# Kernel optimization log

Measured on AMD Instinct MI355X. Metric: run time of the kernel, lower is better.

## Reference

```python
import jax, jax.numpy as jnp
import numpy as np

NLAT, NLON = 361, 720
LMAX = NLAT               # equiangular grid: lmax = nlat
MMAX = NLON // 2 + 1      # mmax = nlon//2 + 1
B, C = 1, 128


def _precompute_legpoly(mmax, lmax, t, csphase=True):
    """Associated Legendre vandermonde P_l^m(cos t), orthonormal, inverse=True
    (norm factor 1 for 'ortho'). Shape [mmax, lmax, nlat]. Setup-time numpy only."""
    x = np.cos(t)
    nmax = max(mmax, lmax)
    vdm = np.zeros((nmax, nmax, len(x)))
    vdm[0, 0] = np.sqrt(1.0 / (4.0 * np.pi))
    for l in range(1, nmax):
        vdm[l - 1, l] = np.sqrt(2 * l + 1) * x * vdm[l - 1, l - 1]
        vdm[l, l] = np.sqrt((2 * l + 1) * (1 + x) * (1 - x) / (2 * l)) * vdm[l - 1, l - 1]
    for l in range(2, nmax):
        for m in range(l - 1):
            a = np.sqrt((2 * l - 1) / (l - m) * (2 * l + 1) / (l + m))
            b = np.sqrt((l + m - 1) / (l - m) * (2 * l + 1) / (2 * l - 3) * (l - m - 1) / (l + m))
            vdm[m, l] = a * x * vdm[m, l - 1] - b * vdm[m, l - 2]
    vdm = vdm[:mmax, :lmax]
    if csphase:
        vdm[1::2] *= -1.0  # Condon-Shortley phase on odd m
    return vdm


def setup_inputs() -> dict:
    key = jax.random.key(0)
    # spherical harmonic coefficients as real view: [B, C, lmax, mmax, 2]
    x_real = jax.random.normal(key, (B, C, LMAX, MMAX, 2), dtype=jnp.float32)
    # equiangular (Clenshaw-Curtiss) colatitudes, t = flip(arccos(cos(pi*j/(n-1))))
    t = np.pi * np.arange(NLAT) / (NLAT - 1)
    pct = jnp.asarray(_precompute_legpoly(MMAX, LMAX, t), dtype=jnp.float32)  # [mmax, lmax, nlat]
    return {"x_real": x_real, "pct": pct}


def reference(x_real, pct):
    # single-device case: comm sizes == 1, all distributed transposes are identity
    # and nlatpad == nlonpad == 0.
    # per-m triangular Legendre contraction over l (torch einsum '...lmr,mlk->...kmr')
    xs = jnp.einsum('bclmr,mlk->bckmr', x_real, pct)        # [B, C, nlat, mmax, 2]
    xc = jax.lax.complex(xs[..., 0], xs[..., 1])            # [B, C, nlat, mmax]
    # inverse real FFT along longitude, norm='forward' (no 1/n scaling on inverse)
    out = jnp.fft.irfft(xc, n=NLON, axis=-1, norm='forward')  # [B, C, nlat, nlon]
    return out.astype(x_real.dtype)
```

## Files before the change

### kernel.cpp

```cpp
#include <hip/hip_runtime.h>
#include <cstddef>

#define CC   128
#define LDIM 361
#define MDIM 361
#define KDIM 361
#define NLON 720
#define LP   384
#define MRP  736
#define NP   768
#define CK   (CC*KDIM)
#define CR   (2*CC)

typedef __attribute__((ext_vector_type(8))) short short8;
typedef __attribute__((ext_vector_type(4))) float floatx4;

__device__ __forceinline__ unsigned short f2bf(float f) {
    union { float f; unsigned u; } v; v.f = f;
    unsigned u = v.u;
    u += 0x7fffu + ((u >> 16) & 1u);
    return (unsigned short)(u >> 16);
}

__device__ __forceinline__ void async_copy16(const void* g, void* l) {
    __builtin_amdgcn_global_load_lds(
        (const __attribute__((address_space(1))) void*)g,
        (__attribute__((address_space(3))) void*)l, 16, 0, 0);
}

__global__ void sht_gen_T(unsigned short* __restrict__ Tp) {
    int idx = blockIdx.x * 256 + threadIdx.x;
    if (idx >= NP * MRP) return;
    int n = idx / MRP, mr = idx - n * MRP;
    float v = 0.f;
    if (n < NLON && mr < 2 * MDIM) {
        int m = mr >> 1, im = mr & 1;
        if (m == 0)            v = im ? 0.f : 1.f;
        else if (m == MDIM-1)  v = im ? 0.f : ((n & 1) ? -1.f : 1.f);
        else {
            int ph = (m * n) % NLON;
            float ang = (float)ph * (float)(3.14159265358979323846 / 360.0);
            v = im ? (-2.f * sinf(ang)) : (2.f * cosf(ang));
        }
    }
    Tp[idx] = f2bf(v);
}

__global__ __launch_bounds__(256)
void sht_prep_x(const float* __restrict__ x, unsigned short* __restrict__ xA) {
    __shared__ float2 tile[64][33];
    const int mt = blockIdx.x;
    const int lt = blockIdx.y;
    const int c  = blockIdx.z;
    const int t  = threadIdx.x;

    #pragma unroll
    for (int u = 0; u < 8; ++u) {
        int p  = t + 256 * u;
        int li = p >> 5, mi = p & 31;
        int l = lt * 64 + li, m = mt * 32 + mi;
        float2 v = make_float2(0.f, 0.f);
        if (l < LDIM && m < MDIM)
            v = *(const float2*)(x + ((size_t)(c * LDIM + l) * MDIM + m) * 2);
        tile[li][mi] = v;
    }
    __syncthreads();

    #pragma unroll
    for (int u = 0; u < 2; ++u) {
        int s  = t + 256 * u;
        int mi = s >> 4, rr = (s >> 3) & 1, lo = (s & 7) * 8;
        int m = mt * 32 + mi;
        if (m >= MDIM) continue;
        short8 h;
        #pragma unroll
        for (int e = 0; e < 8; ++e) {
            float2 p = tile[lo + e][mi];
            h[e] = (short)f2bf(rr ? p.y : p.x);
        }
        *(short8*)(xA + ((size_t)m * CR + 2 * c + rr) * LP + lt * 64 + lo) = h;
    }
}

__global__ __launch_bounds__(256)
void sht_stageA(const float* __restrict__ pct, const unsigned short* __restrict__ xA,
                unsigned short* __restrict__ xs) {
    __shared__ unsigned short As[128 * 32];
    __shared__ unsigned short Bs[32 * 130];

    const int m   = blockIdx.y;
    const int ct  = blockIdx.x & 1;
    const int kt  = blockIdx.x >> 1;
    const int c0  = ct * 128;
    const int n0  = kt * 128;
    const int t   = threadIdx.x;
    const int w   = t >> 6, L = t & 63;
    const int wr  = w & 1, wc = w >> 1;
    const int lane15 = L & 15, quad = L >> 4;
    const int bl = t >> 3, bkq = t & 7;

    const unsigned short* xAm = xA + (size_t)m * CR * LP;
    const float* pctm = pct + (size_t)m * LDIM * KDIM;

    floatx4 acc[4][4] = {};

    for (int kb = 0; kb < LP; kb += 32) {
        #pragma unroll
        for (int i = 0; i < 2; ++i) {
            int s = w * 128 + i * 64 + L;
            int cr = s >> 2, lq = s & 3;
            async_copy16(xAm + (size_t)(c0 + cr) * LP + kb + lq * 8,
                         As + (size_t)(w * 128 + i * 64) * 8);
        }
        {
            int l = kb + bl;
            bool lok = (l < LDIM);
            const float* prow = pctm + (size_t)l * KDIM;
            #pragma unroll
            for (int u = 0; u < 4; ++u) {
                int kc = n0 + u * 32 + bkq * 4;
                float f0 = (lok && kc + 0 < KDIM) ? prow[kc + 0] : 0.f;
                float f1 = (lok && kc + 1 < KDIM) ? prow[kc + 1] : 0.f;
                float f2 = (lok && kc + 2 < KDIM) ? prow[kc + 2] : 0.f;
                float f3 = (lok && kc + 3 < KDIM) ? prow[kc + 3] : 0.f;
                unsigned* bp = (unsigned*)&Bs[bl * 130 + u * 32 + bkq * 4];
                bp[0] = (unsigned)f2bf(f0) | ((unsigned)f2bf(f1) << 16);
                bp[1] = (unsigned)f2bf(f2) | ((unsigned)f2bf(f3) << 16);
            }
        }
        __syncthreads();

        short8 af[4];
        #pragma unroll
        for (int i = 0; i < 4; ++i) {
            int row = wr * 64 + i * 16 + lane15;
            af[i] = *(const short8*)&As[(row * 4 + quad) * 8];
        }
        #pragma unroll
        for (int jf = 0; jf < 4; ++jf) {
            int col = wc * 64 + jf * 16 + lane15;
            short8 bf;
            #pragma unroll
            for (int j = 0; j < 8; ++j)
                bf[j] = (short)Bs[(quad * 8 + j) * 130 + col];
            #pragma unroll
            for (int i = 0; i < 4; ++i)
                acc[i][jf] = __builtin_amdgcn_mfma_f32_16x16x32_bf16(af[i], bf, acc[i][jf], 0, 0, 0);
        }
        __syncthreads();
    }

    #pragma unroll
    for (int i = 0; i < 4; ++i) {
        #pragma unroll
        for (int jf = 0; jf < 4; ++jf) {
            int k = n0 + wc * 64 + jf * 16 + lane15;
            if (k >= KDIM) continue;
            #pragma unroll
            for (int eh = 0; eh < 2; ++eh) {
                int cr = c0 + wr * 64 + i * 16 + quad * 4 + eh * 2;
                int c  = cr >> 1;
                unsigned pack = (unsigned)f2bf(acc[i][jf][eh * 2]) |
                                ((unsigned)f2bf(acc[i][jf][eh * 2 + 1]) << 16);
                *(unsigned*)(xs + (size_t)(c * KDIM + k) * MRP + 2 * m) = pack;
            }
        }
    }
}

__global__ __launch_bounds__(256)
void sht_stageB(const unsigned short* __restrict__ xs, const unsigned short* __restrict__ Tp,
                float* __restrict__ out) {
    __shared__ unsigned short As[128 * 32];
    __shared__ unsigned short Bs[128 * 32];

    const int nt  = blockIdx.x;
    const int ckt = blockIdx.y;
    const int ck0 = ckt * 128, n0 = nt * 128;
    const int t   = threadIdx.x;
    const int w   = t >> 6, L = t & 63;
    const int wr  = w & 1, wc = w >> 1;
    const int lane15 = L & 15, quad = L >> 4;

    floatx4 acc[4][4] = {};

    for (int kb = 0; kb < MRP; kb += 32) {
        #pragma unroll
        for (int i = 0; i < 2; ++i) {
            int s = w * 128 + i * 64 + L;
            int rr = s >> 2, mq = s & 3;
            async_copy16(xs + (size_t)(ck0 + rr) * MRP + kb + mq * 8,
                         As + (size_t)(w * 128 + i * 64) * 8);
            async_copy16(Tp + (size_t)(n0 + rr) * MRP + kb + mq * 8,
                         Bs + (size_t)(w * 128 + i * 64) * 8);
        }
        __syncthreads();

        short8 af[4], bfr[4];
        #pragma unroll
        for (int i = 0; i < 4; ++i)
            af[i] = *(const short8*)&As[((wr * 64 + i * 16 + lane15) * 4 + quad) * 8];
        #pragma unroll
        for (int jf = 0; jf < 4; ++jf)
            bfr[jf] = *(const short8*)&Bs[((wc * 64 + jf * 16 + lane15) * 4 + quad) * 8];
        #pragma unroll
        for (int i = 0; i < 4; ++i)
            #pragma unroll
            for (int jf = 0; jf < 4; ++jf)
                acc[i][jf] = __builtin_amdgcn_mfma_f32_16x16x32_bf16(af[i], bfr[jf], acc[i][jf], 0, 0, 0);
        __syncthreads();
    }

    #pragma unroll
    for (int i = 0; i < 4; ++i) {
        int ckr = ck0 + wr * 64 + i * 16 + quad * 4;
        #pragma unroll
        for (int jf = 0; jf < 4; ++jf) {
            int j = n0 + wc * 64 + jf * 16 + lane15;
            if (j >= NLON) continue;
            #pragma unroll
            for (int e = 0; e < 4; ++e)
                out[(size_t)(ckr + e) * NLON + j] = acc[i][jf][e];
        }
    }
}

extern "C" void kernel_launch(void* const* d_in, const int* in_sizes, int n_in,
                              void* d_out, int out_size, void* d_ws, size_t ws_size,
                              hipStream_t stream) {
    const float* x   = (const float*)d_in[0];
    const float* pct = (const float*)d_in[1];
    float* out = (float*)d_out;

    unsigned short* xs = (unsigned short*)d_ws;
    unsigned short* Tp = xs + (size_t)CK * MRP;
    unsigned short* xA = (unsigned short*)d_out;

    sht_gen_T<<<(NP * MRP + 255) / 256, 256, 0, stream>>>(Tp);
    sht_prep_x<<<dim3(12, 6, 128), 256, 0, stream>>>(x, xA);
    sht_stageA<<<dim3(6, MDIM), 256, 0, stream>>>(pct, xA, xs);
    sht_stageB<<<dim3(6, MDIM), 256, 0, stream>>>(xs, Tp, out);
}
```

Measured before the change: 726.5 us.

## Pre-transpose pct to bf16, enlarge GEMM tiles, and add XCD-aware block swizzle

Adds a kernel that converts pct to bf16 in a K-major padded layout, so stage A can load B tiles with async global-to-LDS copies. Until now each block converted fp32 to bf16 on the fly and read LDS transposed. Stage A and stage B now run 512-thread blocks with 128x384 tiles, so all of K or a large N slice is covered per block and the A operand is reused more. Blocks are remapped with an XCD-aware swizzle so neighbouring tiles share L2. The cost is an extra prep kernel and extra workspace, and the old stage A path is kept as a fallback when the workspace is too small.

Result: faster. 676.0 us (-7.0%).

```diff
diff --git a/kernel.cpp b/kernel.cpp
--- a/kernel.cpp
+++ b/kernel.cpp
@@ -7,6 +7,7 @@
 #define KDIM 361
 #define NLON 720
 #define LP   384
+#define KP   384
 #define MRP  736
 #define NP   768
 #define CK   (CC*KDIM)
@@ -26,6 +27,13 @@
     __builtin_amdgcn_global_load_lds(
         (const __attribute__((address_space(1))) void*)g,
         (__attribute__((address_space(3))) void*)l, 16, 0, 0);
+}
+
+__device__ __forceinline__ int xcd_swz(int id, int P) {
+    int x = id & 7, g = id >> 3;
+    int q = P >> 3, r = P & 7;
+    int start = (x < r) ? x * (q + 1) : r * (q + 1) + (x - r) * q;
+    return start + g;
 }
 
 __global__ void sht_gen_T(unsigned short* __restrict__ Tp) {
@@ -48,7 +56,7 @@
 
 __global__ __launch_bounds__(256)
 void sht_prep_x(const float* __restrict__ x, unsigned short* __restrict__ xA) {
-    __shared__ float2 tile[64][33];
+    __shared__ float tp[2][64 * 33 + 4];
     const int mt = blockIdx.x;
     const int lt = blockIdx.y;
     const int c  = blockIdx.z;
@@ -62,7 +70,8 @@
         float2 v = make_float2(0.f, 0.f);
         if (l < LDIM && m < MDIM)
             v = *(const float2*)(x + ((size_t)(c * LDIM + l) * MDIM + m) * 2);
-        tile[li][mi] = v;
+        tp[0][li * 33 + mi] = v.x;
+        tp[1][li * 33 + mi] = v.y;
     }
     __syncthreads();
 
@@ -72,13 +81,110 @@
         int mi = s >> 4, rr = (s >> 3) & 1, lo = (s & 7) * 8;
         int m = mt * 32 + mi;
         if (m >= MDIM) continue;
+        const float* pl = tp[rr];
         short8 h;
         #pragma unroll
-        for (int e = 0; e < 8; ++e) {
-            float2 p = tile[lo + e][mi];
-            h[e] = (short)f2bf(rr ? p.y : p.x);
-        }
+        for (int e = 0; e < 8; ++e)
+            h[e] = (short)f2bf(pl[(lo + e) * 33 + mi]);
         *(short8*)(xA + ((size_t)m * CR + 2 * c + rr) * LP + lt * 64 + lo) = h;
+    }
+}
+
+__global__ __launch_bounds__(256)
+void sht_prep_pct(const float* __restrict__ pct, unsigned short* __restrict__ pctT) {
+    __shared__ float tile[32][129];
+    const int m  = blockIdx.y;
+    const int bx = blockIdx.x;
+    const int kt = bx % 3, lt = bx / 3;
+    const int l0 = lt * 32, k0 = kt * 128;
+    const int t  = threadIdx.x;
+
+    const int kk = t & 127, lw = t >> 7;
+    #pragma unroll
+    for (int u = 0; u < 16; ++u) {
+        int li = lw + 2 * u;
+        int l = l0 + li, k = k0 + kk;
+        float v = 0.f;
+        if (l < LDIM && k < KDIM)
+            v = pct[((size_t)m * LDIM + l) * KDIM + k];
+        tile[li][kk] = v;
+    }
+    __syncthreads();
+
+    #pragma unroll
+    for (int u = 0; u < 2; ++u) {
+        int s = t + 256 * u;
+        int ko = s >> 2, lo = (s & 3) * 8;
+        short8 h;
+        #pragma unroll
+        for (int e = 0; e < 8; ++e)
+            h[e] = (short)f2bf(tile[lo + e][ko]);
+        *(short8*)(pctT + ((size_t)m * KP + k0 + ko) * LP + l0 + lo) = h;
+    }
+}
+
+__global__ __launch_bounds__(512)
+void sht_stageA2(const unsigned short* __restrict__ pctT, const unsigned short* __restrict__ xA,
+                 unsigned short* __restrict__ xs) {
+    __shared__ unsigned short As[128 * 32];
+    __shared__ unsigned short Bs[384 * 32];
+
+    const int p   = xcd_swz(blockIdx.x, 2 * MDIM);
+    const int m   = p >> 1, ct = p & 1;
+    const int c0  = ct * 128;
+    const int t   = threadIdx.x;
+    const int w   = t >> 6, L = t & 63;
+    const int wr  = w & 1, wc = w >> 1;
+    const int lane15 = L & 15, quad = L >> 4;
+    const int arr = t >> 2, alq = t & 3;
+
+    const unsigned short* xAm = xA + (size_t)m * CR * LP;
+    const unsigned short* pTm = pctT + (size_t)m * KP * LP;
+
+    floatx4 acc[4][6] = {};
+
+    for (int kb = 0; kb < LP; kb += 32) {
+        async_copy16(xAm + (size_t)(c0 + arr) * LP + kb + alq * 8,
+                     As + (size_t)(w * 64) * 8);
+        #pragma unroll
+        for (int u = 0; u < 3; ++u) {
+            int s = u * 512 + t;
+            int rr = s >> 2, lq = s & 3;
+            async_copy16(pTm + (size_t)rr * LP + kb + lq * 8,
+                         Bs + (size_t)(u * 512 + w * 64) * 8);
+        }
+        __syncthreads();
+
+        short8 af[4], bf[6];
+        #pragma unroll
+        for (int i = 0; i < 4; ++i)
+            af[i] = *(const short8*)&As[((wr * 64 + i * 16 + lane15) * 4 + quad) * 8];
+        #pragma unroll
+        for (int j = 0; j < 6; ++j)
+            bf[j] = *(const short8*)&Bs[((wc * 96 + j * 16 + lane15) * 4 + quad) * 8];
+        #pragma unroll
+        for (int i = 0; i < 4; ++i)
+            #pragma unroll
+            for (int j = 0; j < 6; ++j)
+                acc[i][j] = __builtin_amdgcn_mfma_f32_16x16x32_bf16(af[i], bf[j], acc[i][j], 0, 0, 0);
+        __syncthreads();
+    }
+
+    #pragma unroll
+    for (int j = 0; j < 6; ++j) {
+        int k = wc * 96 + j * 16 + lane15;
+        if (k >= KDIM) continue;
+        #pragma unroll
+        for (int i = 0; i < 4; ++i) {
+            #pragma unroll
+            for (int eh = 0; eh < 2; ++eh) {
+                int cr = c0 + wr * 64 + i * 16 + quad * 4 + eh * 2;
+                int c  = cr >> 1;
+                unsigned pack = (unsigned)f2bf(acc[i][j][eh * 2]) |
+                                ((unsigned)f2bf(acc[i][j][eh * 2 + 1]) << 16);
+                *(unsigned*)(xs + (size_t)(c * KDIM + k) * MRP + 2 * m) = pack;
+            }
+        }
     }
 }
 
@@ -168,46 +274,47 @@
     }
 }
 
-__global__ __launch_bounds__(256)
-void sht_stageB(const unsigned short* __restrict__ xs, const unsigned short* __restrict__ Tp,
-                float* __restrict__ out) {
+__global__ __launch_bounds__(512)
+void sht_stageB2(const unsigned short* __restrict__ xs, const unsigned short* __restrict__ Tp,
+                 float* __restrict__ out) {
     __shared__ unsigned short As[128 * 32];
-    __shared__ unsigned short Bs[128 * 32];
-
-    const int nt  = blockIdx.x;
-    const int ckt = blockIdx.y;
-    const int ck0 = ckt * 128, n0 = nt * 128;
+    __shared__ unsigned short Bs[384 * 32];
+
+    const int p   = xcd_swz(blockIdx.x, 2 * MDIM);
+    const int ckt = p >> 1, nt = p & 1;
+    const int ck0 = ckt * 128, n0 = nt * 384;
     const int t   = threadIdx.x;
     const int w   = t >> 6, L = t & 63;
     const int wr  = w & 1, wc = w >> 1;
     const int lane15 = L & 15, quad = L >> 4;
-
-    floatx4 acc[4][4] = {};
+    const int arr = t >> 2, alq = t & 3;
+
+    floatx4 acc[4][6] = {};
 
     for (int kb = 0; kb < MRP; kb += 32) {
-        #pragma unroll
-        for (int i = 0; i < 2; ++i) {
-            int s = w * 128 + i * 64 + L;
-            int rr = s >> 2, mq = s & 3;
-            async_copy16(xs + (size_t)(ck0 + rr) * MRP + kb + mq * 8,
-                         As + (size_t)(w * 128 + i * 64) * 8);
-            async_copy16(Tp + (size_t)(n0 + rr) * MRP + kb + mq * 8,
-                         Bs + (size_t)(w * 128 + i * 64) * 8);
-        }
-        __syncthreads();
-
-        short8 af[4], bfr[4];
+        async_copy16(xs + (size_t)(ck0 + arr) * MRP + kb + alq * 8,
+                     As + (size_t)(w * 64) * 8);
+        #pragma unroll
+        for (int u = 0; u < 3; ++u) {
+            int s = u * 512 + t;
+            int rr = s >> 2, lq = s & 3;
+            async_copy16(Tp + (size_t)(n0 + rr) * MRP + kb + lq * 8,
+                         Bs + (size_t)(u * 512 + w * 64) * 8);
+        }
+        __syncthreads();
+
+        short8 af[4], bf[6];
         #pragma unroll
         for (int i = 0; i < 4; ++i)
             af[i] = *(const short8*)&As[((wr * 64 + i * 16 + lane15) * 4 + quad) * 8];
         #pragma unroll
-        for (int jf = 0; jf < 4; ++jf)
-            bfr[jf] = *(const short8*)&Bs[((wc * 64 + jf * 16 + lane15) * 4 + quad) * 8];
+        for (int j = 0; j < 6; ++j)
+            bf[j] = *(const short8*)&Bs[((wc * 96 + j * 16 + lane15) * 4 + quad) * 8];
         #pragma unroll
         for (int i = 0; i < 4; ++i)
             #pragma unroll
-            for (int jf = 0; jf < 4; ++jf)
-                acc[i][jf] = __builtin_amdgcn_mfma_f32_16x16x32_bf16(af[i], bfr[jf], acc[i][jf], 0, 0, 0);
+            for (int j = 0; j < 6; ++j)
+                acc[i][j] = __builtin_amdgcn_mfma_f32_16x16x32_bf16(af[i], bf[j], acc[i][j], 0, 0, 0);
         __syncthreads();
     }
 
@@ -215,12 +322,12 @@
     for (int i = 0; i < 4; ++i) {
         int ckr = ck0 + wr * 64 + i * 16 + quad * 4;
         #pragma unroll
-        for (int jf = 0; jf < 4; ++jf) {
-            int j = n0 + wc * 64 + jf * 16 + lane15;
-            if (j >= NLON) continue;
+        for (int j = 0; j < 6; ++j) {
+            int jj = n0 + wc * 96 + j * 16 + lane15;
+            if (jj >= NLON) continue;
             #pragma unroll
             for (int e = 0; e < 4; ++e)
-                out[(size_t)(ckr + e) * NLON + j] = acc[i][jf][e];
+                out[(size_t)(ckr + e) * NLON + jj] = acc[i][j][e];
         }
     }
 }
@@ -236,8 +343,18 @@
     unsigned short* Tp = xs + (size_t)CK * MRP;
     unsigned short* xA = (unsigned short*)d_out;
 
+    const size_t base_shorts = (size_t)CK * MRP + (size_t)NP * MRP;
+    const size_t pctT_shorts = (size_t)MDIM * KP * LP;
+    const bool fast = ws_size >= (base_shorts + pctT_shorts) * sizeof(unsigned short);
+
     sht_gen_T<<<(NP * MRP + 255) / 256, 256, 0, stream>>>(Tp);
     sht_prep_x<<<dim3(12, 6, 128), 256, 0, stream>>>(x, xA);
-    sht_stageA<<<dim3(6, MDIM), 256, 0, stream>>>(pct, xA, xs);
-    sht_stageB<<<dim3(6, MDIM), 256, 0, stream>>>(xs, Tp, out);
-}
+    if (fast) {
+        unsigned short* pctT = Tp + (size_t)NP * MRP;
+        sht_prep_pct<<<dim3(36, MDIM), 256, 0, stream>>>(pct, pctT);
+        sht_stageA2<<<dim3(2 * MDIM), 512, 0, stream>>>(pctT, xA, xs);
+    } else {
+        sht_stageA<<<dim3(6, MDIM), 256, 0, stream>>>(pct, xA, xs);
+    }
+    sht_stageB2<<<dim3(2 * MDIM), 512, 0, stream>>>(xs, Tp, out);
+}
```
